# Performance work log

Measured on AMD Instinct MI355X. Metric: run time of the kernel, lower is better.

Reference implementation:

```python
import jax, jax.numpy as jnp
import numpy as np

B, NMAX, D, NUM = 1024, 128, 256, 4
EPS = 1e-8
NEG = -1e9


def segment_softmax(logits, seg):
    # torch_geometric-style softmax over ragged segments. logits: (T,)
    m = jax.ops.segment_max(logits, seg, num_segments=B)
    e = jnp.exp(logits - m[seg])
    s = jax.ops.segment_sum(e, seg, num_segments=B)
    return e / (s[seg] + 1e-16)


def to_dense(v, seg, pos):
    # scatter ragged rows into (B, NMAX, ...) dense batch
    return jnp.zeros((B, NMAX) + v.shape[1:], v.dtype).at[seg, pos].set(v)


def uot_badmm(x, q0d, maskf, a1, a2, a3, rho):
    # Bregman-ADMM solver for entropic unbalanced OT (f_method='badmm-e').
    # x: (B,N,D) cost (to be maximized); q0d, maskf: (B,N,1); a1,a2,a3,rho: (NUM,)
    log_p0 = jnp.full((B, 1, D), -jnp.log(float(D)), x.dtype)  # uniform dim prior
    log_q0 = jnp.log(q0d + EPS)                                # (B,N,1)
    log_t = log_q0 + log_p0                                    # T init = q0 p0^T
    log_s = log_t
    log_mu = log_p0
    log_eta = log_q0
    z = jnp.zeros_like(x)
    z1 = jnp.zeros_like(log_p0)
    z2 = jnp.zeros_like(log_q0)
    neg = (1.0 - maskf) * NEG  # exclude padded rows from N-axis softmax
    for k in range(NUM):
        r, b1, b2, b3 = rho[k], a1[k], a2[k], a3[k]
        # T-update: rows (over D) sum to eta
        y = (x - z + r * log_s) / (b2 + r)
        log_t = log_eta + jax.nn.log_softmax(y, axis=2)
        # S-update: columns (over N) sum to mu, masked
        y = (z + r * log_t) / (b1 + r) + neg
        log_s = log_mu + jax.nn.log_softmax(y, axis=1)
        # unbalanced marginal updates (KL to priors, weight a3)
        log_mu = (b3 * log_p0 - z1 + r * jax.nn.logsumexp(log_s, axis=1, keepdims=True)) / (b3 + r)
        log_eta = (b3 * log_q0 - z2 + r * jax.nn.logsumexp(log_t, axis=2, keepdims=True)) / (b3 + r)
        # dual ascent
        t = jnp.exp(log_t) * maskf
        s = jnp.exp(log_s) * maskf
        z = z + r * (t - s)
        z1 = z1 + r * (jnp.exp(log_mu) - jnp.sum(s, axis=1, keepdims=True))
        z2 = z2 + r * (jnp.exp(log_eta) - jnp.sum(t, axis=2, keepdims=True)) * maskf
    return jnp.exp(log_t) * maskf


def setup_inputs() -> dict:
    rng = np.random.default_rng(0)
    lengths = rng.integers(NMAX // 2, NMAX + 1, size=B)
    lengths[0] = NMAX  # ensure max size present
    batch = jnp.asarray(np.repeat(np.arange(B), lengths), dtype=jnp.int32)
    total = int(lengths.sum())
    ks = jax.random.split(jax.random.key(0), 8)
    x = jax.random.normal(ks[0], (total, D), jnp.float32)
    W1 = jax.random.normal(ks[1], (2 * D, D), jnp.float32) / np.float32(np.sqrt(D))
    W2 = jax.random.normal(ks[2], (1, 2 * D), jnp.float32) / np.float32(np.sqrt(2 * D))
    rho = 0.1 * jax.random.normal(ks[3], (NUM,), jnp.float32)
    a1 = 0.1 * jax.random.normal(ks[4], (NUM,), jnp.float32)
    a2 = 0.1 * jax.random.normal(ks[5], (NUM,), jnp.float32)
    a3 = 0.1 * jax.random.normal(ks[6], (NUM,), jnp.float32)
    return {"x": x, "batch": batch, "W1": W1, "W2": W2, "rho": rho, "a1": a1, "a2": a2, "a3": a3}


def reference(x, batch, W1, W2, rho, a1, a2, a3):
    # attention-based sample prior q0 (q0 != 'fixed' branch)
    h = jnp.tanh(x @ W1.T)          # (T, 2D)
    logits = (h @ W2.T)[:, 0]       # (T,)
    q0 = segment_softmax(logits, batch)[:, None]  # (T, 1)
    # ragged -> dense batch (to_dense_batch)
    counts = jax.ops.segment_sum(jnp.ones_like(batch), batch, num_segments=B)
    starts = jnp.cumsum(counts) - counts
    pos = jnp.arange(batch.shape[0]) - starts[batch]
    xd = to_dense(x, batch, pos)    # (B, NMAX, D)
    q0d = to_dense(q0, batch, pos)  # (B, NMAX, 1)
    mask = to_dense(jnp.ones((batch.shape[0], 1), x.dtype), batch, pos)  # (B, NMAX, 1)
    trans = uot_badmm(xd, q0d, mask,
                      jax.nn.softplus(a1), jax.nn.softplus(a2),
                      jax.nn.softplus(a3), jax.nn.softplus(rho))
    frot = D * xd * trans * mask    # (B, NMAX, D)
    return jnp.sum(frot, axis=1)    # (B, D)
```

## Files before the change

### kernel.cpp

```cpp
#include <hip/hip_runtime.h>
#include <math.h>

#define BB   1024
#define DD   256
#define LOGD 5.5451774444795624753f
#define RST  260

typedef __attribute__((ext_vector_type(8))) short short8;
typedef __attribute__((ext_vector_type(4))) float f32x4;

__device__ __forceinline__ float wave_sum(float v){
  #pragma unroll
  for (int off=32; off>0; off>>=1) v += __shfl_xor(v, off, 64);
  return v;
}
__device__ __forceinline__ float wave_max(float v){
  #pragma unroll
  for (int off=32; off>0; off>>=1) v = fmaxf(v, __shfl_xor(v, off, 64));
  return v;
}
__device__ __forceinline__ float grp_sum(float v){
  v += __shfl_xor(v, 1, 64);
  v += __shfl_xor(v, 2, 64);
  v += __shfl_xor(v, 4, 64);
  v += __shfl_xor(v, 8, 64);
  return v;
}
__device__ __forceinline__ float fast_tanh(float x){
  return 1.0f - 2.0f/(__expf(2.0f*x)+1.0f);
}
__device__ __forceinline__ unsigned short f2bf(float f){
  unsigned int u = __float_as_uint(f);
  unsigned int r = u + 0x7FFFu + ((u >> 16) & 1u);
  return (unsigned short)(r >> 16);
}
__device__ __forceinline__ float decq(int q16){ return (float)q16 * (1.0f/512.0f); }
__device__ __forceinline__ int   zenc(float z){
  float t = fmaf(z, 4096.0f, 12582912.0f);
  return __float_as_int(t) - 0x4B400000;
}
__device__ __forceinline__ float zdec(int q){ return (float)q * (1.0f/4096.0f); }
__device__ __forceinline__ int lo16(unsigned u){ return ((int)(u<<16))>>16; }
__device__ __forceinline__ int hi16(unsigned u){ return ((int)u)>>16; }
__device__ __forceinline__ unsigned pk2(int a, int b){
  return ((unsigned)a & 0xffffu) | ((unsigned)b << 16);
}
__device__ __forceinline__ unsigned pkadd_sat(unsigned a, unsigned b){
  unsigned d; asm("v_pk_add_i16 %0, %1, %2 clamp" : "=v"(d) : "v"(a), "v"(b)); return d;
}

__global__ void k_pre(const float* __restrict__ W1, unsigned short* __restrict__ w1b,
                      const int* __restrict__ batch, int T, int* __restrict__ starts,
                      const float* __restrict__ rho, const float* __restrict__ a1,
                      const float* __restrict__ a2, const float* __restrict__ a3,
                      float* __restrict__ P, float* __restrict__ logits)
{
  const int blk = blockIdx.x, tid = threadIdx.x;
  if (blk < 64){
    const int t = blk*256 + tid;
    #pragma unroll
    for (int i=0;i<2;i++){
      const int idx = (t*2 + i)*4;
      const float4 v = *(const float4*)(W1 + idx);
      *(ushort4*)(w1b + idx) = make_ushort4(f2bf(v.x), f2bf(v.y), f2bf(v.z), f2bf(v.w));
    }
  } else if (blk < 69){
    const int b = (blk-64)*256 + tid;
    if (b <= BB){
      int lo = 0, hi = T;
      while (lo < hi){ int mid = (lo+hi)>>1; if (batch[mid] < b) lo = mid+1; else hi = mid; }
      starts[b] = lo;
    }
  } else if (blk == 69){
    if (tid == 0){
      float lm = -LOGD, z1 = 0.f;
      for (int k=0;k<4;k++){
        float r  = log1pf(expf(rho[k]));
        float b1 = log1pf(expf(a1[k]));
        float b2 = log1pf(expf(a2[k]));
        float b3 = log1pf(expf(a3[k]));
        P[k]    = r;
        P[4+k]  = 1.f/(b1+r);
        P[8+k]  = 1.f/(b2+r);
        P[12+k] = lm;
        P[16+k] = b3;
        P[20+k] = 1.f/(b3+r);
        float lmn = (b3*(-LOGD) - z1 + r*lm)/(b3+r);
        z1 += r*(expf(lmn)-expf(lm));
        lm = lmn;
      }
    }
  } else {
    const int i = (blk-70)*1024 + tid*4;
    if (i + 3 < T){
      *(float4*)(logits + i) = make_float4(0.f,0.f,0.f,0.f);
    } else {
      for (int j=0; j<4 && i+j < T; j++) logits[i+j] = 0.f;
    }
  }
}

#define LPW 72
__global__ __launch_bounds__(512, 2) void k_mlp(
    const float* __restrict__ x, const unsigned short* __restrict__ w1b,
    const float* __restrict__ W2, float* __restrict__ logits, int T)
{
  __shared__ unsigned short Xs[128*LPW];
  __shared__ unsigned short Ws[128*LPW];
  __shared__ float lred[128];
  const int by = blockIdx.x;
  const int bx = blockIdx.y;
  const int tid = threadIdx.x;
  if (tid < 128) lred[tid] = 0.f;

  const int l = tid & 63;
  const int w = tid >> 6;
  const int wm = w >> 2;
  const int wn = w & 3;
  const int lr = l & 15, quad = l >> 4;
  const int srow = tid >> 2;
  const int sseg = tid & 3;
  const int wrow = tid >> 3;
  const int wseg = tid & 7;

  f32x4 acc[4][2];
  #pragma unroll
  for (int mi=0;mi<4;mi++)
    #pragma unroll
    for (int ni=0;ni<2;ni++) acc[mi][ni] = (f32x4){0.f,0.f,0.f,0.f};

  for (int kt=0; kt<4; kt++){
    const int k0 = kt*64;
    {
      const int grow = bx*128 + srow;
      #pragma unroll
      for (int i=0;i<4;i++){
        float4 v = make_float4(0.f,0.f,0.f,0.f);
        if (grow < T) v = *(const float4*)(x + (size_t)grow*DD + k0 + sseg*16 + i*4);
        *(ushort4*)&Xs[srow*LPW + sseg*16 + i*4] =
            make_ushort4(f2bf(v.x), f2bf(v.y), f2bf(v.z), f2bf(v.w));
      }
    }
    #pragma unroll
    for (int h=0; h<2; h++){
      const int r = h*64 + wrow;
      *(short8*)&Ws[r*LPW + wseg*8] =
          *(const short8*)(w1b + (size_t)(by*128 + r)*DD + k0 + wseg*8);
    }
    __syncthreads();
    #pragma unroll
    for (int ks=0; ks<2; ks++){
      short8 afr[4], bfr[2];
      #pragma unroll
      for (int mi=0;mi<4;mi++)
        afr[mi] = *(const short8*)&Xs[(wm*64 + mi*16 + lr)*LPW + ks*32 + quad*8];
      #pragma unroll
      for (int ni=0;ni<2;ni++)
        bfr[ni] = *(const short8*)&Ws[(wn*32 + ni*16 + lr)*LPW + ks*32 + quad*8];
      #pragma unroll
      for (int mi=0;mi<4;mi++)
        #pragma unroll
        for (int ni=0;ni<2;ni++)
          acc[mi][ni] = __builtin_amdgcn_mfma_f32_16x16x32_bf16(afr[mi], bfr[ni], acc[mi][ni], 0, 0, 0);
    }
    __syncthreads();
  }

  float w2v[2];
  #pragma unroll
  for (int ni=0;ni<2;ni++) w2v[ni] = W2[by*128 + wn*32 + ni*16 + lr];
  #pragma unroll
  for (int mi=0;mi<4;mi++){
    float p[4];
    #pragma unroll
    for (int v=0; v<4; v++){
      p[v] = fast_tanh(acc[mi][0][v])*w2v[0] + fast_tanh(acc[mi][1][v])*w2v[1];
      #pragma unroll
      for (int off=1; off<16; off<<=1) p[v] += __shfl_xor(p[v], off, 64);
    }
    if (lr == 0){
      #pragma unroll
      for (int v=0; v<4; v++)
        atomicAdd(&lred[wm*64 + mi*16 + quad*4 + v], p[v]);
    }
  }
  __syncthreads();
  if (tid < 128){
    const int grow = bx*128 + tid;
    if (grow < T) atomicAdd(logits + grow, lred[tid]);
  }
}

__global__ __launch_bounds__(512, 2) void k_solver(
    const float* __restrict__ x, const float* __restrict__ logits,
    const int* __restrict__ starts, const float* __restrict__ P,
    float* __restrict__ out)
{
  __shared__ __align__(16) float red[32*RST];
  __shared__ __align__(16) float colv[DD];
  const int b = blockIdx.x;
  const int start = starts[b];
  const int len = starts[b+1] - start;
  const int tid = threadIdx.x;
  const int w = tid >> 6, l = tid & 63;
  const int sub = l >> 4;
  const int c0  = l & 15;
  const int n0 = w*16;
  int nv = len - n0; nv = nv < 0 ? 0 : (nv > 16 ? 16 : nv);

  const float r0=P[0], r1=P[1], r2=P[2], r3=P[3];
  const float i10=P[4], i11=P[5], i12=P[6];
  const float i20=P[8], i21=P[9], i22=P[10], i23=P[11];
  const float mu0=P[12], mu1=P[13], mu2=P[14];
  const float b30=P[16], b31=P[17], b32=P[18];
  const float e30=P[20], e31=P[21], e32=P[22];

  const float* lg = logits + start;
  float v0 = (l      < len) ? lg[l]    : -3.0e38f;
  float v1 = (l+64   < len) ? lg[l+64] : -3.0e38f;
  float sm = wave_max(fmaxf(v0,v1));
  float se0 = (l    < len) ? __expf(v0-sm) : 0.f;
  float se1 = (l+64 < len) ? __expf(v1-sm) : 0.f;
  float ssum0 = wave_sum(se0+se1);
  const float sinv = 1.f/(ssum0 + 1e-16f);
  const float esel = (n0 < 64) ? se0 : se1;

  float slqg[4], etag[4], z2g[4];
  uint2 ap[4][4];
  uint2 zp[4][4];
  #pragma unroll
  for (int g=0; g<4; g++){
    const int row = n0 + 4*g + sub;
    const float ev = __shfl(esel, row & 63, 64);
    const float lq = __logf(ev*sinv + 1e-8f);
    slqg[g] = lq; etag[g] = lq; z2g[g] = 0.f;
    #pragma unroll
    for (int q=0;q<4;q++){ zp[g][q].x = 0u; zp[g][q].y = 0u; }
  }

  const float* xbase = x + (size_t)(start + n0 + sub)*DD + 4*c0;

  {
    float sp[16];
    #pragma unroll
    for (int j=0;j<16;j++) sp[j]=0.f;
    #pragma unroll
    for (int g=0; g<4; g++){
      if (4*g + sub < nv){
        const float* xp = xbase + (size_t)(4*g)*DD;
        const float a0 = slqg[g] - LOGD;
        float ss = 0.f;
        #pragma unroll
        for (int q=0;q<4;q++){
          const float4 xv = *(const float4*)(xp + 64*q);
          const float xvv[4] = {xv.x, xv.y, xv.z, xv.w};
          int ny[4];
          #pragma unroll
          for (int j=0;j<4;j++){
            const float y = (xvv[j] + r0*a0) * i20;
            ss += __expf(y);
            ny[j] = __float2int_rn(y*512.f);
          }
          ap[g][q].x = pk2(ny[0],ny[1]);
          ap[g][q].y = pk2(ny[2],ny[3]);
        }
        ss = grp_sum(ss);
        const float off = etag[g] - __logf(ss);
        const int offi = __float2int_rn(fmaxf(off, -56.f)*512.f);
        const unsigned offpk = pk2(offi, offi);
        #pragma unroll
        for (int q=0;q<4;q++){
          ap[g][q].x = pkadd_sat(ap[g][q].x, offpk);
          ap[g][q].y = pkadd_sat(ap[g][q].y, offpk);
          sp[4*q+0] += __expf((r0*decq(lo16(ap[g][q].x))) * i10);
          sp[4*q+1] += __expf((r0*decq(hi16(ap[g][q].x))) * i10);
          sp[4*q+2] += __expf((r0*decq(lo16(ap[g][q].y))) * i10);
          sp[4*q+3] += __expf((r0*decq(hi16(ap[g][q].y))) * i10);
        }
        const float en = (b30*slqg[g] - z2g[g] + r0*etag[g]) * e30;
        z2g[g] += r0*(__expf(en) - __expf(etag[g]));
        etag[g] = en;
      }
    }
    #pragma unroll
    for (int q=0;q<4;q++)
      *(float4*)&red[(4*w+sub)*RST + 64*q + 4*c0] =
          make_float4(sp[4*q], sp[4*q+1], sp[4*q+2], sp[4*q+3]);
  }
  __syncthreads();
  if (tid < DD){
    float s = 0.f;
    #pragma unroll
    for (int i=0;i<32;i++) s += red[i*RST + tid];
    colv[tid] = __logf(s);
  }
  __syncthreads();

  #pragma unroll
  for (int k=1;k<3;k++){
    const float rkm = (k==1)? r0 : r1;
    const float ib1m= (k==1)? i10 : i11;
    const float mum = (k==1)? mu0 : mu1;
    const float rk  = (k==1)? r1 : r2;
    const float ib1k= (k==1)? i11 : i12;
    const float ib2k= (k==1)? i21 : i22;
    const float b3k = (k==1)? b31 : b32;
    const float e3k = (k==1)? e31 : e32;
    float sp[16];
    #pragma unroll
    for (int j=0;j<16;j++) sp[j]=0.f;
    #pragma unroll
    for (int g=0; g<4; g++){
      if (4*g + sub < nv){
        const float* xp = xbase + (size_t)(4*g)*DD;
        float ss = 0.f;
        #pragma unroll
        for (int q=0;q<4;q++){
          const float4 lscq = *(const float4*)&colv[64*q + 4*c0];
          const float4 xv   = *(const float4*)(xp + 64*q);
          const float xvv[4]  = {xv.x, xv.y, xv.z, xv.w};
          const float lscv[4] = {lscq.x, lscq.y, lscq.z, lscq.w};
          const int aq[4] = {lo16(ap[g][q].x), hi16(ap[g][q].x),
                             lo16(ap[g][q].y), hi16(ap[g][q].y)};
          const int zq[4] = {lo16(zp[g][q].x), hi16(zp[g][q].x),
                             lo16(zp[g][q].y), hi16(zp[g][q].y)};
          int ny[4], nz[4];
          #pragma unroll
          for (int j=0;j<4;j++){
            const float lt = decq(aq[j]);
            float zf = zdec(zq[j]);
            const float ys  = (zf + rkm*lt) * ib1m;
            const float lsn = mum + ys - lscv[j];
            zf += rkm*(__expf(lt) - __expf(lsn));
            nz[j] = zenc(zf);
            const float y = (xvv[j] - zdec(nz[j]) + rk*lsn) * ib2k;
            ss += __expf(y);
            ny[j] = __float2int_rn(y*512.f);
          }
          ap[g][q].x = pk2(ny[0],ny[1]);
          ap[g][q].y = pk2(ny[2],ny[3]);
          zp[g][q].x = pk2(nz[0],nz[1]);
          zp[g][q].y = pk2(nz[2],nz[3]);
        }
        ss = grp_sum(ss);
        const float off = etag[g] - __logf(ss);
        const int offi = __float2int_rn(fmaxf(off, -56.f)*512.f);
        const unsigned offpk = pk2(offi, offi);
        #pragma unroll
        for (int q=0;q<4;q++){
          ap[g][q].x = pkadd_sat(ap[g][q].x, offpk);
          ap[g][q].y = pkadd_sat(ap[g][q].y, offpk);
          sp[4*q+0] += __expf((zdec(lo16(zp[g][q].x)) + rk*decq(lo16(ap[g][q].x))) * ib1k);
          sp[4*q+1] += __expf((zdec(hi16(zp[g][q].x)) + rk*decq(hi16(ap[g][q].x))) * ib1k);
          sp[4*q+2] += __expf((zdec(lo16(zp[g][q].y)) + rk*decq(lo16(ap[g][q].y))) * ib1k);
          sp[4*q+3] += __expf((zdec(hi16(zp[g][q].y)) + rk*decq(hi16(ap[g][q].y))) * ib1k);
        }
        const float en = (b3k*slqg[g] - z2g[g] + rk*etag[g]) * e3k;
        z2g[g] += rk*(__expf(en) - __expf(etag[g]));
        etag[g] = en;
      }
    }
    #pragma unroll
    for (int q=0;q<4;q++)
      *(float4*)&red[(4*w+sub)*RST + 64*q + 4*c0] =
          make_float4(sp[4*q], sp[4*q+1], sp[4*q+2], sp[4*q+3]);
    __syncthreads();
    if (tid < DD){
      float s = 0.f;
      #pragma unroll
      for (int i=0;i<32;i++) s += red[i*RST + tid];
      colv[tid] = __logf(s);
    }
    __syncthreads();
  }

  {
    float op[16];
    #pragma unroll
    for (int j=0;j<16;j++) op[j]=0.f;
    #pragma unroll
    for (int g=0; g<4; g++){
      if (4*g + sub < nv){
        const float* xp = xbase + (size_t)(4*g)*DD;
        float ey[16];
        float ss = 0.f;
        #pragma unroll
        for (int q=0;q<4;q++){
          const float4 lscq = *(const float4*)&colv[64*q + 4*c0];
          const float4 xv   = *(const float4*)(xp + 64*q);
          const float xvv[4]  = {xv.x, xv.y, xv.z, xv.w};
          const float lscv[4] = {lscq.x, lscq.y, lscq.z, lscq.w};
          const int aq[4] = {lo16(ap[g][q].x), hi16(ap[g][q].x),
                             lo16(ap[g][q].y), hi16(ap[g][q].y)};
          const int zq[4] = {lo16(zp[g][q].x), hi16(zp[g][q].x),
                             lo16(zp[g][q].y), hi16(zp[g][q].y)};
          #pragma unroll
          for (int j=0;j<4;j++){
            const float lt = decq(aq[j]);
            float zf = zdec(zq[j]);
            const float ys  = (zf + r2*lt) * i12;
            const float lsn = mu2 + ys - lscv[j];
            zf += r2*(__expf(lt) - __expf(lsn));
            const float y = (xvv[j] - zf + r3*lsn) * i23;
            const float e = __expf(y);
            ey[4*q+j] = e;
            ss += e;
          }
        }
        ss = grp_sum(ss);
        const float rs = __expf(etag[g]) / ss;
        #pragma unroll
        for (int q=0;q<4;q++){
          const float4 xv = *(const float4*)(xp + 64*q);
          op[4*q+0] += xv.x * ey[4*q+0] * rs;
          op[4*q+1] += xv.y * ey[4*q+1] * rs;
          op[4*q+2] += xv.z * ey[4*q+2] * rs;
          op[4*q+3] += xv.w * ey[4*q+3] * rs;
        }
      }
    }
    #pragma unroll
    for (int q=0;q<4;q++)
      *(float4*)&red[(4*w+sub)*RST + 64*q + 4*c0] =
          make_float4(op[4*q], op[4*q+1], op[4*q+2], op[4*q+3]);
    __syncthreads();
    if (tid < DD){
      float s = 0.f;
      #pragma unroll
      for (int i=0;i<32;i++) s += red[i*RST + tid];
      out[(size_t)b*DD + tid] = 256.0f * s;
    }
  }
}

extern "C" void kernel_launch(void* const* d_in, const int* in_sizes, int n_in,
                              void* d_out, int out_size, void* d_ws, size_t ws_size,
                              hipStream_t stream) {
  const float* x    = (const float*)d_in[0];
  const int*   batch= (const int*)d_in[1];
  const float* W1   = (const float*)d_in[2];
  const float* W2   = (const float*)d_in[3];
  const float* rho  = (const float*)d_in[4];
  const float* a1   = (const float*)d_in[5];
  const float* a2   = (const float*)d_in[6];
  const float* a3   = (const float*)d_in[7];
  float* out = (float*)d_out;
  const int T = in_sizes[1];

  float* logits = (float*)d_ws;
  int*   starts = (int*)(logits + T);
  float* P      = (float*)(starts + 1028);
  unsigned short* w1b = (unsigned short*)(P + 32);

  const int zb = (T + 1023) / 1024;
  k_pre<<<70 + zb, 256, 0, stream>>>(W1, w1b, batch, T, starts, rho, a1, a2, a3, P, logits);
  k_mlp<<<dim3(4, (T+127)/128), 512, 0, stream>>>(x, w1b, W2, logits, T);
  k_solver<<<BB, 512, 0, stream>>>(x, logits, starts, P, out);
}
```

Baseline: 363.3 us.

## Double solver block size to 1024 threads with 8 rows per wave

The solver now launches 1024 threads per batch element, so each wave handles 8 rows instead of 16, which halves the per-thread register state for the packed T and Z arrays. Partial column sums are built per column chunk rather than kept in 16-wide accumulators. The final pass recomputes the exponentials instead of buffering them in registers. Together these aim to cut register pressure and add more waves to hide latency. In exchange the shared reduction buffer doubles to 64 rows and the column reduction does twice as many adds, and the last phase repeats the exp work and the global x reads.

```diff
diff --git a/kernel.cpp b/kernel.cpp
--- a/kernel.cpp
+++ b/kernel.cpp
@@ -191,12 +191,12 @@
   }
 }
 
-__global__ __launch_bounds__(512, 2) void k_solver(
+__global__ __launch_bounds__(1024, 8) void k_solver(
     const float* __restrict__ x, const float* __restrict__ logits,
     const int* __restrict__ starts, const float* __restrict__ P,
     float* __restrict__ out)
 {
-  __shared__ __align__(16) float red[32*RST];
+  __shared__ __align__(16) float red[64*RST];
   __shared__ __align__(16) float colv[DD];
   const int b = blockIdx.x;
   const int start = starts[b];
@@ -205,8 +205,8 @@
   const int w = tid >> 6, l = tid & 63;
   const int sub = l >> 4;
   const int c0  = l & 15;
-  const int n0 = w*16;
-  int nv = len - n0; nv = nv < 0 ? 0 : (nv > 16 ? 16 : nv);
+  const int n0 = w*8;
+  int nv = len - n0; nv = nv < 0 ? 0 : (nv > 8 ? 8 : nv);
 
   const float r0=P[0], r1=P[1], r2=P[2], r3=P[3];
   const float i10=P[4], i11=P[5], i12=P[6];
@@ -225,11 +225,11 @@
   const float sinv = 1.f/(ssum0 + 1e-16f);
   const float esel = (n0 < 64) ? se0 : se1;
 
-  float slqg[4], etag[4], z2g[4];
-  uint2 ap[4][4];
-  uint2 zp[4][4];
-  #pragma unroll
-  for (int g=0; g<4; g++){
+  float slqg[2], etag[2], z2g[2];
+  uint2 ap[2][4];
+  uint2 zp[2][4];
+  #pragma unroll
+  for (int g=0; g<2; g++){
     const int row = n0 + 4*g + sub;
     const float ev = __shfl(esel, row & 63, 64);
     const float lq = __logf(ev*sinv + 1e-8f);
@@ -239,13 +239,12 @@
   }
 
   const float* xbase = x + (size_t)(start + n0 + sub)*DD + 4*c0;
+  const int rr = (4*w + sub)*RST + 4*c0;
 
   {
-    float sp[16];
-    #pragma unroll
-    for (int j=0;j<16;j++) sp[j]=0.f;
-    #pragma unroll
-    for (int g=0; g<4; g++){
+    unsigned offpk[2] = {0u, 0u};
+    #pragma unroll
+    for (int g=0; g<2; g++){
       if (4*g + sub < nv){
         const float* xp = xbase + (size_t)(4*g)*DD;
         const float a0 = slqg[g] - LOGD;
@@ -267,31 +266,34 @@
         ss = grp_sum(ss);
         const float off = etag[g] - __logf(ss);
         const int offi = __float2int_rn(fmaxf(off, -56.f)*512.f);
-        const unsigned offpk = pk2(offi, offi);
-        #pragma unroll
-        for (int q=0;q<4;q++){
-          ap[g][q].x = pkadd_sat(ap[g][q].x, offpk);
-          ap[g][q].y = pkadd_sat(ap[g][q].y, offpk);
-          sp[4*q+0] += __expf((r0*decq(lo16(ap[g][q].x))) * i10);
-          sp[4*q+1] += __expf((r0*decq(hi16(ap[g][q].x))) * i10);
-          sp[4*q+2] += __expf((r0*decq(lo16(ap[g][q].y))) * i10);
-          sp[4*q+3] += __expf((r0*decq(hi16(ap[g][q].y))) * i10);
-        }
+        offpk[g] = pk2(offi, offi);
         const float en = (b30*slqg[g] - z2g[g] + r0*etag[g]) * e30;
         z2g[g] += r0*(__expf(en) - __expf(etag[g]));
         etag[g] = en;
       }
     }
     #pragma unroll
-    for (int q=0;q<4;q++)
-      *(float4*)&red[(4*w+sub)*RST + 64*q + 4*c0] =
-          make_float4(sp[4*q], sp[4*q+1], sp[4*q+2], sp[4*q+3]);
+    for (int q=0;q<4;q++){
+      float sp4[4] = {0.f,0.f,0.f,0.f};
+      #pragma unroll
+      for (int g=0; g<2; g++){
+        if (4*g + sub < nv){
+          ap[g][q].x = pkadd_sat(ap[g][q].x, offpk[g]);
+          ap[g][q].y = pkadd_sat(ap[g][q].y, offpk[g]);
+          sp4[0] += __expf((r0*decq(lo16(ap[g][q].x))) * i10);
+          sp4[1] += __expf((r0*decq(hi16(ap[g][q].x))) * i10);
+          sp4[2] += __expf((r0*decq(lo16(ap[g][q].y))) * i10);
+          sp4[3] += __expf((r0*decq(hi16(ap[g][q].y))) * i10);
+        }
+      }
+      *(float4*)&red[rr + 64*q] = make_float4(sp4[0], sp4[1], sp4[2], sp4[3]);
+    }
   }
   __syncthreads();
   if (tid < DD){
     float s = 0.f;
     #pragma unroll
-    for (int i=0;i<32;i++) s += red[i*RST + tid];
+    for (int i=0;i<64;i++) s += red[i*RST + tid];
     colv[tid] = __logf(s);
   }
   __syncthreads();
@@ -306,11 +308,9 @@
     const float ib2k= (k==1)? i21 : i22;
     const float b3k = (k==1)? b31 : b32;
     const float e3k = (k==1)? e31 : e32;
-    float sp[16];
-    #pragma unroll
-    for (int j=0;j<16;j++) sp[j]=0.f;
-    #pragma unroll
-    for (int g=0; g<4; g++){
+    unsigned offpk[2] = {0u, 0u};
+    #pragma unroll
+    for (int g=0; g<2; g++){
       if (4*g + sub < nv){
         const float* xp = xbase + (size_t)(4*g)*DD;
         float ss = 0.f;
@@ -345,44 +345,44 @@
         ss = grp_sum(ss);
         const float off = etag[g] - __logf(ss);
         const int offi = __float2int_rn(fmaxf(off, -56.f)*512.f);
-        const unsigned offpk = pk2(offi, offi);
-        #pragma unroll
-        for (int q=0;q<4;q++){
-          ap[g][q].x = pkadd_sat(ap[g][q].x, offpk);
-          ap[g][q].y = pkadd_sat(ap[g][q].y, offpk);
-          sp[4*q+0] += __expf((zdec(lo16(zp[g][q].x)) + rk*decq(lo16(ap[g][q].x))) * ib1k);
-          sp[4*q+1] += __expf((zdec(hi16(zp[g][q].x)) + rk*decq(hi16(ap[g][q].x))) * ib1k);
-          sp[4*q+2] += __expf((zdec(lo16(zp[g][q].y)) + rk*decq(lo16(ap[g][q].y))) * ib1k);
-          sp[4*q+3] += __expf((zdec(hi16(zp[g][q].y)) + rk*decq(hi16(ap[g][q].y))) * ib1k);
-        }
+        offpk[g] = pk2(offi, offi);
         const float en = (b3k*slqg[g] - z2g[g] + rk*etag[g]) * e3k;
         z2g[g] += rk*(__expf(en) - __expf(etag[g]));
         etag[g] = en;
       }
     }
     #pragma unroll
-    for (int q=0;q<4;q++)
-      *(float4*)&red[(4*w+sub)*RST + 64*q + 4*c0] =
-          make_float4(sp[4*q], sp[4*q+1], sp[4*q+2], sp[4*q+3]);
+    for (int q=0;q<4;q++){
+      float sp4[4] = {0.f,0.f,0.f,0.f};
+      #pragma unroll
+      for (int g=0; g<2; g++){
+        if (4*g + sub < nv){
+          ap[g][q].x = pkadd_sat(ap[g][q].x, offpk[g]);
+          ap[g][q].y = pkadd_sat(ap[g][q].y, offpk[g]);
+          sp4[0] += __expf((zdec(lo16(zp[g][q].x)) + rk*decq(lo16(ap[g][q].x))) * ib1k);
+          sp4[1] += __expf((zdec(hi16(zp[g][q].x)) + rk*decq(hi16(ap[g][q].x))) * ib1k);
+          sp4[2] += __expf((zdec(lo16(zp[g][q].y)) + rk*decq(lo16(ap[g][q].y))) * ib1k);
+          sp4[3] += __expf((zdec(hi16(zp[g][q].y)) + rk*decq(hi16(ap[g][q].y))) * ib1k);
+        }
+      }
+      *(float4*)&red[rr + 64*q] = make_float4(sp4[0], sp4[1], sp4[2], sp4[3]);
+    }
     __syncthreads();
     if (tid < DD){
       float s = 0.f;
       #pragma unroll
-      for (int i=0;i<32;i++) s += red[i*RST + tid];
+      for (int i=0;i<64;i++) s += red[i*RST + tid];
       colv[tid] = __logf(s);
     }
     __syncthreads();
   }
 
   {
-    float op[16];
-    #pragma unroll
-    for (int j=0;j<16;j++) op[j]=0.f;
-    #pragma unroll
-    for (int g=0; g<4; g++){
+    float rs[2] = {0.f, 0.f};
+    #pragma unroll
+    for (int g=0; g<2; g++){
       if (4*g + sub < nv){
         const float* xp = xbase + (size_t)(4*g)*DD;
-        float ey[16];
         float ss = 0.f;
         #pragma unroll
         for (int q=0;q<4;q++){
@@ -402,32 +402,46 @@
             const float lsn = mu2 + ys - lscv[j];
             zf += r2*(__expf(lt) - __expf(lsn));
             const float y = (xvv[j] - zf + r3*lsn) * i23;
-            const float e = __expf(y);
-            ey[4*q+j] = e;
-            ss += e;
+            ss += __expf(y);
           }
         }
         ss = grp_sum(ss);
-        const float rs = __expf(etag[g]) / ss;
-        #pragma unroll
-        for (int q=0;q<4;q++){
-          const float4 xv = *(const float4*)(xp + 64*q);
-          op[4*q+0] += xv.x * ey[4*q+0] * rs;
-          op[4*q+1] += xv.y * ey[4*q+1] * rs;
-          op[4*q+2] += xv.z * ey[4*q+2] * rs;
-          op[4*q+3] += xv.w * ey[4*q+3] * rs;
-        }
-      }
-    }
-    #pragma unroll
-    for (int q=0;q<4;q++)
-      *(float4*)&red[(4*w+sub)*RST + 64*q + 4*c0] =
-          make_float4(op[4*q], op[4*q+1], op[4*q+2], op[4*q+3]);
+        rs[g] = __expf(etag[g]) / ss;
+      }
+    }
+    #pragma unroll
+    for (int q=0;q<4;q++){
+      float op4[4] = {0.f,0.f,0.f,0.f};
+      const float4 lscq = *(const float4*)&colv[64*q + 4*c0];
+      const float lscv[4] = {lscq.x, lscq.y, lscq.z, lscq.w};
+      #pragma unroll
+      for (int g=0; g<2; g++){
+        if (4*g + sub < nv){
+          const float4 xv = *(const float4*)(xbase + (size_t)(4*g)*DD + 64*q);
+          const float xvv[4] = {xv.x, xv.y, xv.z, xv.w};
+          const int aq[4] = {lo16(ap[g][q].x), hi16(ap[g][q].x),
+                             lo16(ap[g][q].y), hi16(ap[g][q].y)};
+          const int zq[4] = {lo16(zp[g][q].x), hi16(zp[g][q].x),
+                             lo16(zp[g][q].y), hi16(zp[g][q].y)};
+          #pragma unroll
+          for (int j=0;j<4;j++){
+            const float lt = decq(aq[j]);
+            float zf = zdec(zq[j]);
+            const float ys  = (zf + r2*lt) * i12;
+            const float lsn = mu2 + ys - lscv[j];
+            zf += r2*(__expf(lt) - __expf(lsn));
+            const float y = (xvv[j] - zf + r3*lsn) * i23;
+            op4[j] += xvv[j] * __expf(y) * rs[g];
+          }
+        }
+      }
+      *(float4*)&red[rr + 64*q] = make_float4(op4[0], op4[1], op4[2], op4[3]);
+    }
     __syncthreads();
     if (tid < DD){
       float s = 0.f;
       #pragma unroll
-      for (int i=0;i<32;i++) s += red[i*RST + tid];
+      for (int i=0;i<64;i++) s += red[i*RST + tid];
       out[(size_t)b*DD + tid] = 256.0f * s;
     }
   }
@@ -455,5 +469,5 @@
   const int zb = (T + 1023) / 1024;
   k_pre<<<70 + zb, 256, 0, stream>>>(W1, w1b, batch, T, starts, rho, a1, a2, a3, P, logits);
   k_mlp<<<dim3(4, (T+127)/128), 512, 0, stream>>>(x, w1b, W2, logits, T);
-  k_solver<<<BB, 512, 0, stream>>>(x, logits, starts, P, out);
-}
+  k_solver<<<BB, 1024, 0, stream>>>(x, logits, starts, P, out);
+}
```

Result: slower. 595.1 us (+63.8%).
